# Performance work log

Hardware: AMD Instinct MI355X
Metric: run time of the kernel (lower is better)

Reference implementation:

```python
import jax, jax.numpy as jnp
from jax import lax
import numpy as np

# Quantization constants (would come from the torch state dict)
IN_S = 1.0 / 255.0   # input_scale
IN_ZP = 0            # input_zp
W_S  = [0.02, 0.02, 0.02, 0.02, 0.02, 0.02, 0.02]   # per-layer w_scale
W_ZP = [128, 128, 128, 128, 128, 128, 128]           # per-layer w_zp
OUT_S  = [0.05, 0.04, 0.04, 0.04, 0.04, 0.04, 0.05]  # per-layer act out_scale
OUT_ZP = [0, 0, 0, 0, 0, 0, 0]
PADS = [2, 0, 1, 1, 1, 1, 0]
WT_SCALE = 0.02  # last_part.w_scale used to dequantize the transpose-conv weight
DN = ('NCHW', 'OIHW', 'NCHW')


def qconv(x, w, b, in_s, in_zp, w_s, w_zp, out_s, out_zp, pad):
    # fake-quantize activation to uint8 range, shift by zero point
    xq = jnp.clip(jnp.round(x / in_s) + in_zp, 0.0, 255.0) - in_zp
    wq = w.astype(jnp.float32) - w_zp
    y = lax.conv_general_dilated(xq, wq, (1, 1), [(pad, pad), (pad, pad)],
                                 dimension_numbers=DN)
    y = y + b.astype(jnp.float32)[None, :, None, None]   # int32 accumulator bias
    # requantize to int8 range, dequantize, relu
    yq = jnp.clip(jnp.round(y * (in_s * w_s / out_s)), -127.0, 127.0)
    return jax.nn.relu((yq - out_zp) * out_s)


def deconv(x, wt):
    # torch ConvTranspose2d(16,1,k=9,stride=4,padding=4,bias=False)
    # equivalent: lhs-dilated conv with flipped, transposed kernel, pad = k-1-p = 4
    k = jnp.flip(jnp.transpose(wt, (1, 0, 2, 3)), axis=(2, 3))  # (O=1, I=16, 9, 9)
    return lax.conv_general_dilated(x, k, (1, 1), [(4, 4), (4, 4)],
                                    lhs_dilation=(4, 4), dimension_numbers=DN)


def setup_inputs() -> dict:
    key = jax.random.key(0)
    ks = jax.random.split(key, 20)
    shapes_w = [(16, 1, 5, 5), (12, 16, 1, 1), (12, 12, 3, 3), (12, 12, 3, 3),
                (12, 12, 3, 3), (12, 12, 3, 3), (16, 12, 1, 1)]
    inp = {"x": jax.random.uniform(ks[0], (16, 1, 512, 512), dtype=jnp.float32)}
    for i, sh in enumerate(shapes_w):
        inp[f"w{i}"] = jax.random.randint(ks[1 + i], sh, 0, 256, dtype=jnp.int32)
        inp[f"b{i}"] = jax.random.randint(ks[8 + i], (sh[0],), 0, 512, dtype=jnp.int32)
    # dequantized transpose-conv weight: int8-ish values * w_scale
    inp["wt"] = jax.random.normal(ks[15], (16, 1, 9, 9), dtype=jnp.float32) * WT_SCALE
    return inp


def reference(x, w0, w1, w2, w3, w4, w5, w6,
              b0, b1, b2, b3, b4, b5, b6, wt):
    ws = [w0, w1, w2, w3, w4, w5, w6]
    bs = [b0, b1, b2, b3, b4, b5, b6]
    cur_s, cur_zp = IN_S, IN_ZP
    for i in range(7):
        x = qconv(x, ws[i], bs[i], cur_s, cur_zp,
                  W_S[i], W_ZP[i], OUT_S[i], OUT_ZP[i], PADS[i])
        cur_s, cur_zp = OUT_S[i], OUT_ZP[i]
    return deconv(x, wt)
```

## Files before the change

### kernel.cpp

```cpp
#include <hip/hip_runtime.h>
#include <stdint.h>

typedef unsigned int uint;
typedef float f2 __attribute__((ext_vector_type(2)));
#define DEV __device__ __forceinline__


DEV int dot4(uint a, uint b, int c) {
#if __has_builtin(__builtin_amdgcn_sdot4)
    return __builtin_amdgcn_sdot4((int)a, (int)b, c, false);
#else
    int r = c;
    r += (int)(int8_t)(a)       * (int)(int8_t)(b);
    r += (int)(int8_t)(a >> 8)  * (int)(int8_t)(b >> 8);
    r += (int)(int8_t)(a >> 16) * (int)(int8_t)(b >> 16);
    r += (int)(int8_t)(a >> 24) * (int)(int8_t)(b >> 24);
    return r;
#endif
}

DEV uint alignbyte(uint hi, uint lo, int m) {
#if __has_builtin(__builtin_amdgcn_alignbyte)
    return __builtin_amdgcn_alignbyte(hi, lo, m);
#else
    return (uint)((((uint64_t)hi << 32) | (uint64_t)lo) >> (8 * m));
#endif
}

DEV uint requant_relu(int acc, float M) {
    float q = rintf((float)acc * M);
    q = fminf(fmaxf(q, -127.f), 127.f);
    q = fmaxf(q, 0.f);
    return (uint)q;
}

__global__ __launch_bounds__(256) void k_quant(const float* __restrict__ x,
                                               uint8_t* __restrict__ xq,
                                               float in_s) {
    int i = blockIdx.x * 256 + threadIdx.x;
    float4 v = ((const float4*)x)[i];
    uint b0 = (uint)fminf(fmaxf(rintf(v.x / in_s), 0.f), 255.f);
    uint b1 = (uint)fminf(fmaxf(rintf(v.y / in_s), 0.f), 255.f);
    uint b2 = (uint)fminf(fmaxf(rintf(v.z / in_s), 0.f), 255.f);
    uint b3 = (uint)fminf(fmaxf(rintf(v.w / in_s), 0.f), 255.f);
    ((uint*)xq)[i] = b0 | (b1 << 8) | (b2 << 16) | (b3 << 24);
}

__global__ __launch_bounds__(256) void k_l0(const uint8_t* __restrict__ xq,
                                            const int* __restrict__ w,
                                            const int* __restrict__ b,
                                            uint8_t* __restrict__ out, float M) {
    __shared__ uint tin[5][68];
    __shared__ uint wrow[5][16];
    __shared__ uint w4p[16];
    __shared__ int  w44[16];
    __shared__ int  beff[16];
    int t  = threadIdx.x;
    int x0 = blockIdx.x * 256;
    int y  = blockIdx.y;
    int n  = blockIdx.z;
    const uint8_t* xp = xq + (size_t)n * 512 * 512;

    for (int j = t; j < 330; j += 256) {
        int r = j / 66, d = j % 66;
        int yy = y - 2 + r;
        int gb = x0 - 4 + 4 * d;
        uint v = 0;
        if ((unsigned)yy < 512u && (unsigned)gb < 512u)
            v = *(const uint*)(xp + (size_t)yy * 512 + gb);
        tin[r][d] = v;
    }
    if (t < 80) {
        int oc = t / 5, r = t % 5;
        uint pk = 0;
#pragma unroll
        for (int k = 0; k < 4; ++k) {
            int wv = w[oc * 25 + r * 5 + k] - 128;
            pk |= ((uint)(uint8_t)(int8_t)wv) << (8 * k);
        }
        wrow[r][oc] = pk;
    }
    if (t < 16) {
        uint pk = 0;
#pragma unroll
        for (int r = 0; r < 4; ++r) {
            int wv = w[t * 25 + r * 5 + 4] - 128;
            pk |= ((uint)(uint8_t)(int8_t)wv) << (8 * r);
        }
        w4p[t] = pk;
        w44[t] = w[t * 25 + 24] - 128;
        int s = 0;
        for (int p = 0; p < 25; ++p) s += w[t * 25 + p] - 128;
        beff[t] = b[t] + 128 * s;
    }
    __syncthreads();

    int m  = (t + 2) & 3;
    int d0 = (t + 2) >> 2;
    uint e0[5], t4[5];
#pragma unroll
    for (int r = 0; r < 5; ++r) {
        uint a0 = tin[r][d0], a1 = tin[r][d0 + 1];
        e0[r] = alignbyte(a1, a0, m) ^ 0x80808080u;
        t4[r] = (a1 >> (8 * m)) & 0xffu;
    }
    uint lo4 = (t4[0] | (t4[1] << 8) | (t4[2] << 16) | (t4[3] << 24)) ^ 0x80808080u;
    int  e44 = (int)(int8_t)(uint8_t)(t4[4] ^ 0x80u);

    int acc[16];
#pragma unroll
    for (int oc = 0; oc < 16; ++oc) acc[oc] = beff[oc];
#pragma unroll
    for (int r = 0; r < 5; ++r)
#pragma unroll
        for (int oc = 0; oc < 16; ++oc) acc[oc] = dot4(e0[r], wrow[r][oc], acc[oc]);
#pragma unroll
    for (int oc = 0; oc < 16; ++oc) {
        acc[oc] = dot4(lo4, w4p[oc], acc[oc]);
        acc[oc] += e44 * w44[oc];
    }

    uint dw[4];
#pragma unroll
    for (int g = 0; g < 4; ++g) {
        uint d = 0;
#pragma unroll
        for (int k = 0; k < 4; ++k) d |= requant_relu(acc[g * 4 + k], M) << (8 * k);
        dw[g] = d;
    }
    size_t pix = (size_t)(n * 512 + y) * 512 + (x0 + t);
    ((uint4*)out)[pix] = make_uint4(dw[0], dw[1], dw[2], dw[3]);
}

template <int IC, int OC>
__global__ __launch_bounds__(256) void k_1x1(const uint8_t* __restrict__ in,
                                             const int* __restrict__ w,
                                             const int* __restrict__ b,
                                             uint8_t* __restrict__ out, float M) {
    constexpr int ICD = IC / 4;
    constexpr int OCD = OC / 4;
    __shared__ uint wl[OC * ICD];
    __shared__ int  bl[OC];
    int t = threadIdx.x;
    for (int j = t; j < OC * ICD; j += 256) {
        int oc = j / ICD, d = j % ICD;
        uint pk = 0;
#pragma unroll
        for (int k = 0; k < 4; ++k) {
            int wv = w[oc * IC + d * 4 + k] - 128;
            pk |= ((uint)(uint8_t)(int8_t)wv) << (8 * k);
        }
        wl[j] = pk;
    }
    if (t < OC) bl[t] = b[t];
    __syncthreads();
    size_t pix = (size_t)blockIdx.x * 256 + t;
    uint a[ICD];
#pragma unroll
    for (int d = 0; d < ICD; ++d) a[d] = ((const uint*)in)[pix * ICD + d];
    uint dws[OCD];
#pragma unroll
    for (int g = 0; g < OCD; ++g) {
        uint dword = 0;
#pragma unroll
        for (int k = 0; k < 4; ++k) {
            int oc = g * 4 + k;
            int acc = bl[oc];
#pragma unroll
            for (int d = 0; d < ICD; ++d) acc = dot4(a[d], wl[oc * ICD + d], acc);
            dword |= requant_relu(acc, M) << (8 * k);
        }
        dws[g] = dword;
    }
#pragma unroll
    for (int g = 0; g < OCD; ++g) ((uint*)out)[pix * OCD + g] = dws[g];
}

__global__ __launch_bounds__(128) void k_3x3(const uint8_t* __restrict__ in,
                                             const int* __restrict__ w,
                                             const int* __restrict__ b,
                                             uint8_t* __restrict__ out, float M) {
    __shared__ uint wl[324];
    __shared__ int  bl[12];
    int t = threadIdx.x;
    for (int j = t; j < 324; j += 128) {
        int pos = j / 36;
        int oc  = (j % 36) / 3;
        int d   = j % 3;
        uint pk = 0;
#pragma unroll
        for (int k = 0; k < 4; ++k) {
            int ic = d * 4 + k;
            int wv = w[oc * 108 + ic * 9 + pos] - 128;
            pk |= ((uint)(uint8_t)(int8_t)wv) << (8 * k);
        }
        wl[j] = pk;
    }
    if (t < 12) bl[t] = b[t];
    __syncthreads();

    int y = blockIdx.x, n = blockIdx.y;
    int x0 = t * 4;
    const uint* ip = (const uint*)in;

    uint inr[3][6][3];
#pragma unroll
    for (int r = 0; r < 3; ++r) {
        int yy = y - 1 + r;
        bool yok = (unsigned)yy < 512u;
#pragma unroll
        for (int cidx = 0; cidx < 6; ++cidx) {
            int xx = x0 - 1 + cidx;
            bool ok = yok && (unsigned)xx < 512u;
            size_t base = ((size_t)(n * 512 + yy) * 512 + xx) * 3;
#pragma unroll
            for (int d = 0; d < 3; ++d) inr[r][cidx][d] = ok ? ip[base + d] : 0u;
        }
    }

    int acc[4][12];
#pragma unroll
    for (int p = 0; p < 4; ++p)
#pragma unroll
        for (int oc = 0; oc < 12; ++oc) acc[p][oc] = bl[oc];

#pragma unroll
    for (int ry = 0; ry < 3; ++ry) {
#pragma unroll
        for (int rx = 0; rx < 3; ++rx) {
            int pos = ry * 3 + rx;
            const uint4* wq = (const uint4*)&wl[pos * 36];
#pragma unroll
            for (int g = 0; g < 3; ++g) {
                uint4 wA = wq[g * 3 + 0];
                uint4 wB = wq[g * 3 + 1];
                uint4 wC = wq[g * 3 + 2];
                uint wocd[4][3] = {{wA.x, wA.y, wA.z}, {wA.w, wB.x, wB.y},
                                   {wB.z, wB.w, wC.x}, {wC.y, wC.z, wC.w}};
#pragma unroll
                for (int k = 0; k < 4; ++k) {
                    int oc = g * 4 + k;
#pragma unroll
                    for (int p = 0; p < 4; ++p) {
                        acc[p][oc] = dot4(inr[ry][rx + p][0], wocd[k][0], acc[p][oc]);
                        acc[p][oc] = dot4(inr[ry][rx + p][1], wocd[k][1], acc[p][oc]);
                        acc[p][oc] = dot4(inr[ry][rx + p][2], wocd[k][2], acc[p][oc]);
                    }
                }
            }
        }
    }

#pragma unroll
    for (int p = 0; p < 4; ++p) {
        uint dws[3];
#pragma unroll
        for (int g = 0; g < 3; ++g) {
            uint dword = 0;
#pragma unroll
            for (int k = 0; k < 4; ++k) dword |= requant_relu(acc[p][g * 4 + k], M) << (8 * k);
            dws[g] = dword;
        }
        size_t pix = (size_t)(n * 512 + y) * 512 + (x0 + p);
        uint* op = (uint*)out;
        op[pix * 3 + 0] = dws[0];
        op[pix * 3 + 1] = dws[1];
        op[pix * 3 + 2] = dws[2];
    }
}

__global__ __launch_bounds__(256) void k_wprep(const float* __restrict__ wt,
                                               float* __restrict__ wp) {
    int idx = blockIdx.x * 256 + threadIdx.x;
    if (idx < 2304) {
        int o = idx & 15, c = (idx >> 4) & 15, pos = idx >> 8;
        int r = pos / 3, s = pos % 3;
        int py = o >> 2, px = o & 3;
        int jy = 4 * r - py, jx = 4 * s - px;
        float v = 0.f;
        if (jy >= 0 && jy < 9 && jx >= 0 && jx < 9)
            v = wt[c * 81 + (8 - jy) * 9 + (8 - jx)];
        wp[idx] = v;
    } else if (idx < 2496) {
        int i2 = idx - 2304;
        int r = i2 >> 6, c = (i2 >> 2) & 15, py = i2 & 3;
        int jy = 4 * r - py;
        float v = 0.f;
        if (jy >= 0 && jy < 9)
            v = wt[c * 81 + (8 - jy) * 9 + 8];
        wp[idx] = v;
    }
}

template <bool ALLPY>
DEV void dc_row5(const float* __restrict__ wrow,
                 const float* __restrict__ w0tab,
                 const uint4* w3, f2* accA, f2* accB) {
    {
        uint wv[4] = {w3[0].x, w3[0].y, w3[0].z, w3[0].w};
#pragma unroll
        for (int c = 0; c < 16; ++c) {
            float x = (float)((wv[c >> 2] >> ((c & 3) * 8)) & 0xffu);
            if (ALLPY) {
                float4 w = *(const float4*)(w0tab + c * 4);
                accA[0].x = fmaf(w.x, x, accA[0].x);
                accA[1].x = fmaf(w.y, x, accA[1].x);
                accA[2].x = fmaf(w.z, x, accA[2].x);
                accA[3].x = fmaf(w.w, x, accA[3].x);
            } else {
                accA[0].x = fmaf(w0tab[c * 4], x, accA[0].x);
            }
        }
    }
#pragma unroll
    for (int s = 1; s < 3; ++s) {
        const float* wb = wrow + s * 256;
        uint wv[4] = {w3[s].x, w3[s].y, w3[s].z, w3[s].w};
#pragma unroll
        for (int c = 0; c < 16; ++c) {
            float x = (float)((wv[c >> 2] >> ((c & 3) * 8)) & 0xffu);
            f2 xx = {x, x};
#pragma unroll
            for (int py = 0; py < (ALLPY ? 4 : 1); ++py) {
                float4 w = *(const float4*)(wb + c * 16 + py * 4);
                f2 wlo = {w.x, w.y};
                f2 whi = {w.z, w.w};
                accA[py] = __builtin_elementwise_fma(wlo, xx, accA[py]);
                accB[py] = __builtin_elementwise_fma(whi, xx, accB[py]);
            }
        }
    }
}

__global__ __launch_bounds__(256, 2) void k_deconv5(const uint8_t* __restrict__ in,
                                                    const float* __restrict__ wp,
                                                    float* __restrict__ out,
                                                    float out_s) {
    __shared__ float wl[2304];
    __shared__ float wl0[192];
    int t = threadIdx.x;
#pragma unroll
    for (int j = 0; j < 9; ++j) wl[j * 256 + t] = wp[j * 256 + t];
    if (t < 192) wl0[t] = wp[2304 + t];
    __syncthreads();

    int tx = blockIdx.x * 256 + t;
    int ty = blockIdx.y;
    int n  = blockIdx.z;
    const uint4* ip = (const uint4*)in + (size_t)n * 512 * 512;

    f2 accA[4], accB[4];
#pragma unroll
    for (int i = 0; i < 4; ++i) { accA[i] = (f2){0.f, 0.f}; accB[i] = (f2){0.f, 0.f}; }

    {
        int iy = ty - 1;
        uint4 w3[3];
#pragma unroll
        for (int s = 0; s < 3; ++s) {
            int ix = tx - 1 + s;
            bool ok = (iy >= 0) && ((unsigned)ix < 512u);
            w3[s] = ok ? ip[(size_t)iy * 512 + ix] : make_uint4(0u, 0u, 0u, 0u);
        }
        dc_row5<false>(&wl[0], &wl0[0], w3, accA, accB);
    }
#pragma unroll 1
    for (int r = 1; r < 3; ++r) {
        int iy = ty - 1 + r;
        uint4 w3[3];
#pragma unroll
        for (int s = 0; s < 3; ++s) {
            int ix = tx - 1 + s;
            bool ok = (iy < 512) && ((unsigned)ix < 512u);
            w3[s] = ok ? ip[(size_t)iy * 512 + ix] : make_uint4(0u, 0u, 0u, 0u);
        }
        dc_row5<true>(&wl[r * 768], &wl0[r * 64], w3, accA, accB);
    }

    int oy0 = 4 * ty, ox0 = 4 * tx;
    float* op = out + (size_t)n * 2045 * 2045;
    int xlim = 2045 - ox0; if (xlim > 4) xlim = 4;
#pragma unroll
    for (int py = 0; py < 4; ++py) {
        int oy = oy0 + py;
        if (oy >= 2045) break;
        size_t rb = (size_t)oy * 2045 + ox0;
        float va[4] = {accA[py].x * out_s, accA[py].y * out_s,
                       accB[py].x * out_s, accB[py].y * out_s};
#pragma unroll
        for (int px = 0; px < 4; ++px) {
            if (px >= xlim) break;
            op[rb + px] = va[px];
        }
    }
}

extern "C" void kernel_launch(void* const* d_in, const int* in_sizes, int n_in,
                              void* d_out, int out_size, void* d_ws, size_t ws_size,
                              hipStream_t stream) {
    const float* x  = (const float*)d_in[0];
    const int*   w0 = (const int*)d_in[1];
    const int*   b0 = (const int*)d_in[2];
    const int*   w1 = (const int*)d_in[3];
    const int*   b1 = (const int*)d_in[4];
    const int*   w2 = (const int*)d_in[5];
    const int*   b2 = (const int*)d_in[6];
    const int*   w3 = (const int*)d_in[7];
    const int*   b3 = (const int*)d_in[8];
    const int*   w4 = (const int*)d_in[9];
    const int*   b4 = (const int*)d_in[10];
    const int*   w5 = (const int*)d_in[11];
    const int*   b5 = (const int*)d_in[12];
    const int*   w6 = (const int*)d_in[13];
    const int*   b6 = (const int*)d_in[14];
    const float* wt = (const float*)d_in[15];
    float* out = (float*)d_out;

    uint8_t* A  = (uint8_t*)d_ws;
    uint8_t* B  = (uint8_t*)d_ws + (size_t)(64 << 20);
    uint8_t* xq = B;
    float*  wpD = (float*)(B + (size_t)(60 << 20));

    const float M0  = (float)((1.0 / 255.0) * 0.02 / 0.05);
    const float M1  = (float)(0.05 * 0.02 / 0.04);
    const float M25 = (float)(0.04 * 0.02 / 0.04);
    const float M6  = (float)(0.04 * 0.02 / 0.05);
    const float IN_S_F = (float)(1.0 / 255.0);

    k_wprep<<<10, 256, 0, stream>>>(wt, wpD);
    k_quant<<<4096, 256, 0, stream>>>(x, xq, IN_S_F);
    k_l0<<<dim3(2, 512, 16), 256, 0, stream>>>(xq, w0, b0, A, M0);
    k_1x1<16, 12><<<16384, 256, 0, stream>>>(A, w1, b1, B, M1);
    k_3x3<<<dim3(512, 16), 128, 0, stream>>>(B, w2, b2, A, M25);
    k_3x3<<<dim3(512, 16), 128, 0, stream>>>(A, w3, b3, B, M25);
    k_3x3<<<dim3(512, 16), 128, 0, stream>>>(B, w4, b4, A, M25);
    k_3x3<<<dim3(512, 16), 128, 0, stream>>>(A, w5, b5, B, M25);
    k_1x1<12, 16><<<16384, 256, 0, stream>>>(B, w6, b6, A, M6);
    k_deconv5<<<dim3(2, 512, 16), 256, 0, stream>>>(A, wpD, out, 0.05f);
}
```

Before: 559.3 us.

## Fuse 1x1 convs into neighbouring kernels and widen deconv per-thread tile

The first 1x1 conv is folded into the 5x5 layer-0 kernel, and the final 1x1 conv is folded into the last 3x3 kernel through a template flag. This removes two launches and two full intermediate activation round trips through global memory. The transpose-conv kernel now has each thread compute two adjacent input columns, giving 8 output pixels per row. That reuses overlapping input loads and halves the grid, at the cost of higher register pressure.

```diff
diff --git a/kernel.cpp b/kernel.cpp
--- a/kernel.cpp
+++ b/kernel.cpp
@@ -27,6 +27,8 @@
 #endif
 }
 
+DEV float bytef(uint v, int k) { return (float)((v >> (8 * k)) & 0xffu); }
+
 DEV uint requant_relu(int acc, float M) {
     float q = rintf((float)acc * M);
     q = fminf(fmaxf(q, -127.f), 127.f);
@@ -49,12 +51,16 @@
 __global__ __launch_bounds__(256) void k_l0(const uint8_t* __restrict__ xq,
                                             const int* __restrict__ w,
                                             const int* __restrict__ b,
-                                            uint8_t* __restrict__ out, float M) {
+                                            uint8_t* __restrict__ out, float M,
+                                            const int* __restrict__ w1,
+                                            const int* __restrict__ b1, float M1) {
     __shared__ uint tin[5][68];
     __shared__ uint wrow[5][16];
     __shared__ uint w4p[16];
     __shared__ int  w44[16];
     __shared__ int  beff[16];
+    __shared__ uint w1l[48];
+    __shared__ int  b1l[12];
     int t  = threadIdx.x;
     int x0 = blockIdx.x * 256;
     int y  = blockIdx.y;
@@ -93,6 +99,17 @@
         for (int p = 0; p < 25; ++p) s += w[t * 25 + p] - 128;
         beff[t] = b[t] + 128 * s;
     }
+    if (t < 48) {
+        int oc = t >> 2, d = t & 3;
+        uint pk = 0;
+#pragma unroll
+        for (int k = 0; k < 4; ++k) {
+            int wv = w1[oc * 16 + d * 4 + k] - 128;
+            pk |= ((uint)(uint8_t)(int8_t)wv) << (8 * k);
+        }
+        w1l[t] = pk;
+    }
+    if (t >= 64 && t < 76) b1l[t - 64] = b1[t - 64];
     __syncthreads();
 
     int m  = (t + 2) & 3;
@@ -128,60 +145,35 @@
         for (int k = 0; k < 4; ++k) d |= requant_relu(acc[g * 4 + k], M) << (8 * k);
         dw[g] = d;
     }
+
     size_t pix = (size_t)(n * 512 + y) * 512 + (x0 + t);
-    ((uint4*)out)[pix] = make_uint4(dw[0], dw[1], dw[2], dw[3]);
-}
-
-template <int IC, int OC>
-__global__ __launch_bounds__(256) void k_1x1(const uint8_t* __restrict__ in,
-                                             const int* __restrict__ w,
-                                             const int* __restrict__ b,
-                                             uint8_t* __restrict__ out, float M) {
-    constexpr int ICD = IC / 4;
-    constexpr int OCD = OC / 4;
-    __shared__ uint wl[OC * ICD];
-    __shared__ int  bl[OC];
-    int t = threadIdx.x;
-    for (int j = t; j < OC * ICD; j += 256) {
-        int oc = j / ICD, d = j % ICD;
-        uint pk = 0;
-#pragma unroll
-        for (int k = 0; k < 4; ++k) {
-            int wv = w[oc * IC + d * 4 + k] - 128;
-            pk |= ((uint)(uint8_t)(int8_t)wv) << (8 * k);
-        }
-        wl[j] = pk;
-    }
-    if (t < OC) bl[t] = b[t];
-    __syncthreads();
-    size_t pix = (size_t)blockIdx.x * 256 + t;
-    uint a[ICD];
-#pragma unroll
-    for (int d = 0; d < ICD; ++d) a[d] = ((const uint*)in)[pix * ICD + d];
-    uint dws[OCD];
-#pragma unroll
-    for (int g = 0; g < OCD; ++g) {
+    uint* op = (uint*)out;
+#pragma unroll
+    for (int g = 0; g < 3; ++g) {
         uint dword = 0;
 #pragma unroll
         for (int k = 0; k < 4; ++k) {
             int oc = g * 4 + k;
-            int acc = bl[oc];
-#pragma unroll
-            for (int d = 0; d < ICD; ++d) acc = dot4(a[d], wl[oc * ICD + d], acc);
-            dword |= requant_relu(acc, M) << (8 * k);
-        }
-        dws[g] = dword;
-    }
-#pragma unroll
-    for (int g = 0; g < OCD; ++g) ((uint*)out)[pix * OCD + g] = dws[g];
-}
-
+            int a2 = b1l[oc];
+#pragma unroll
+            for (int d = 0; d < 4; ++d) a2 = dot4(dw[d], w1l[oc * 4 + d], a2);
+            dword |= requant_relu(a2, M1) << (8 * k);
+        }
+        op[pix * 3 + g] = dword;
+    }
+}
+
+template <bool FUSE>
 __global__ __launch_bounds__(128) void k_3x3(const uint8_t* __restrict__ in,
                                              const int* __restrict__ w,
                                              const int* __restrict__ b,
-                                             uint8_t* __restrict__ out, float M) {
+                                             uint8_t* __restrict__ out, float M,
+                                             const int* __restrict__ w6,
+                                             const int* __restrict__ b6, float M6) {
     __shared__ uint wl[324];
     __shared__ int  bl[12];
+    __shared__ uint w6l[48];
+    __shared__ int  b6l[16];
     int t = threadIdx.x;
     for (int j = t; j < 324; j += 128) {
         int pos = j / 36;
@@ -197,6 +189,19 @@
         wl[j] = pk;
     }
     if (t < 12) bl[t] = b[t];
+    if (FUSE) {
+        if (t >= 16 && t < 64) {
+            int j = t - 16, oc = j / 3, d = j % 3;
+            uint pk = 0;
+#pragma unroll
+            for (int k = 0; k < 4; ++k) {
+                int wv = w6[oc * 12 + d * 4 + k] - 128;
+                pk |= ((uint)(uint8_t)(int8_t)wv) << (8 * k);
+            }
+            w6l[j] = pk;
+        }
+        if (t >= 64 && t < 80) b6l[t - 64] = b6[t - 64];
+    }
     __syncthreads();
 
     int y = blockIdx.x, n = blockIdx.y;
@@ -262,10 +267,28 @@
             dws[g] = dword;
         }
         size_t pix = (size_t)(n * 512 + y) * 512 + (x0 + p);
-        uint* op = (uint*)out;
-        op[pix * 3 + 0] = dws[0];
-        op[pix * 3 + 1] = dws[1];
-        op[pix * 3 + 2] = dws[2];
+        if (!FUSE) {
+            uint* op = (uint*)out;
+            op[pix * 3 + 0] = dws[0];
+            op[pix * 3 + 1] = dws[1];
+            op[pix * 3 + 2] = dws[2];
+        } else {
+            uint dw2[4];
+#pragma unroll
+            for (int g = 0; g < 4; ++g) {
+                uint dword = 0;
+#pragma unroll
+                for (int k = 0; k < 4; ++k) {
+                    int oc = g * 4 + k;
+                    int a2 = b6l[oc];
+#pragma unroll
+                    for (int d = 0; d < 3; ++d) a2 = dot4(dws[d], w6l[oc * 3 + d], a2);
+                    dword |= requant_relu(a2, M6) << (8 * k);
+                }
+                dw2[g] = dword;
+            }
+            ((uint4*)out)[pix] = make_uint4(dw2[0], dw2[1], dw2[2], dw2[3]);
+        }
     }
 }
 
@@ -293,46 +316,57 @@
 }
 
 template <bool ALLPY>
-DEV void dc_row5(const float* __restrict__ wrow,
+DEV void dc_row6(const float* __restrict__ wrow,
                  const float* __restrict__ w0tab,
-                 const uint4* w3, f2* accA, f2* accB) {
-    {
-        uint wv[4] = {w3[0].x, w3[0].y, w3[0].z, w3[0].w};
-#pragma unroll
-        for (int c = 0; c < 16; ++c) {
-            float x = (float)((wv[c >> 2] >> ((c & 3) * 8)) & 0xffu);
-            if (ALLPY) {
-                float4 w = *(const float4*)(w0tab + c * 4);
-                accA[0].x = fmaf(w.x, x, accA[0].x);
-                accA[1].x = fmaf(w.y, x, accA[1].x);
-                accA[2].x = fmaf(w.z, x, accA[2].x);
-                accA[3].x = fmaf(w.w, x, accA[3].x);
-            } else {
-                accA[0].x = fmaf(w0tab[c * 4], x, accA[0].x);
-            }
+                 const uint4* ld,
+                 f2 (&accA)[2][4], f2 (&accB)[2][4]) {
+    uint bv[4][4];
+#pragma unroll
+    for (int s = 0; s < 4; ++s) { bv[s][0] = ld[s].x; bv[s][1] = ld[s].y; bv[s][2] = ld[s].z; bv[s][3] = ld[s].w; }
+#pragma unroll
+    for (int c = 0; c < 16; ++c) {
+        float xA = bytef(bv[0][c >> 2], c & 3);
+        float xB = bytef(bv[1][c >> 2], c & 3);
+        if (ALLPY) {
+            float4 wv = *(const float4*)(w0tab + c * 4);
+            accA[0][0].x = fmaf(wv.x, xA, accA[0][0].x);
+            accA[0][1].x = fmaf(wv.y, xA, accA[0][1].x);
+            accA[0][2].x = fmaf(wv.z, xA, accA[0][2].x);
+            accA[0][3].x = fmaf(wv.w, xA, accA[0][3].x);
+            accA[1][0].x = fmaf(wv.x, xB, accA[1][0].x);
+            accA[1][1].x = fmaf(wv.y, xB, accA[1][1].x);
+            accA[1][2].x = fmaf(wv.z, xB, accA[1][2].x);
+            accA[1][3].x = fmaf(wv.w, xB, accA[1][3].x);
+        } else {
+            float w0 = w0tab[c * 4];
+            accA[0][0].x = fmaf(w0, xA, accA[0][0].x);
+            accA[1][0].x = fmaf(w0, xB, accA[1][0].x);
         }
     }
 #pragma unroll
     for (int s = 1; s < 3; ++s) {
         const float* wb = wrow + s * 256;
-        uint wv[4] = {w3[s].x, w3[s].y, w3[s].z, w3[s].w};
 #pragma unroll
         for (int c = 0; c < 16; ++c) {
-            float x = (float)((wv[c >> 2] >> ((c & 3) * 8)) & 0xffu);
-            f2 xx = {x, x};
+            float xA = bytef(bv[s][c >> 2], c & 3);
+            float xB = bytef(bv[s + 1][c >> 2], c & 3);
+            f2 xxA = {xA, xA};
+            f2 xxB = {xB, xB};
 #pragma unroll
             for (int py = 0; py < (ALLPY ? 4 : 1); ++py) {
-                float4 w = *(const float4*)(wb + c * 16 + py * 4);
-                f2 wlo = {w.x, w.y};
-                f2 whi = {w.z, w.w};
-                accA[py] = __builtin_elementwise_fma(wlo, xx, accA[py]);
-                accB[py] = __builtin_elementwise_fma(whi, xx, accB[py]);
+                float4 wv = *(const float4*)(wb + c * 16 + py * 4);
+                f2 wlo = {wv.x, wv.y};
+                f2 whi = {wv.z, wv.w};
+                accA[0][py] = __builtin_elementwise_fma(wlo, xxA, accA[0][py]);
+                accB[0][py] = __builtin_elementwise_fma(whi, xxA, accB[0][py]);
+                accA[1][py] = __builtin_elementwise_fma(wlo, xxB, accA[1][py]);
+                accB[1][py] = __builtin_elementwise_fma(whi, xxB, accB[1][py]);
             }
         }
     }
 }
 
-__global__ __launch_bounds__(256, 2) void k_deconv5(const uint8_t* __restrict__ in,
+__global__ __launch_bounds__(256, 2) void k_deconv6(const uint8_t* __restrict__ in,
                                                     const float* __restrict__ wp,
                                                     float* __restrict__ out,
                                                     float out_s) {
@@ -344,51 +378,55 @@
     if (t < 192) wl0[t] = wp[2304 + t];
     __syncthreads();
 
-    int tx = blockIdx.x * 256 + t;
+    int gx = t;
     int ty = blockIdx.y;
     int n  = blockIdx.z;
     const uint4* ip = (const uint4*)in + (size_t)n * 512 * 512;
 
-    f2 accA[4], accB[4];
-#pragma unroll
-    for (int i = 0; i < 4; ++i) { accA[i] = (f2){0.f, 0.f}; accB[i] = (f2){0.f, 0.f}; }
+    f2 accA[2][4], accB[2][4];
+#pragma unroll
+    for (int k = 0; k < 2; ++k)
+#pragma unroll
+        for (int i = 0; i < 4; ++i) { accA[k][i] = (f2){0.f, 0.f}; accB[k][i] = (f2){0.f, 0.f}; }
 
     {
         int iy = ty - 1;
-        uint4 w3[3];
-#pragma unroll
-        for (int s = 0; s < 3; ++s) {
-            int ix = tx - 1 + s;
+        uint4 ld[4];
+#pragma unroll
+        for (int s = 0; s < 4; ++s) {
+            int ix = 2 * gx - 1 + s;
             bool ok = (iy >= 0) && ((unsigned)ix < 512u);
-            w3[s] = ok ? ip[(size_t)iy * 512 + ix] : make_uint4(0u, 0u, 0u, 0u);
-        }
-        dc_row5<false>(&wl[0], &wl0[0], w3, accA, accB);
+            ld[s] = ok ? ip[(size_t)iy * 512 + ix] : make_uint4(0u, 0u, 0u, 0u);
+        }
+        dc_row6<false>(&wl[0], &wl0[0], ld, accA, accB);
     }
 #pragma unroll 1
     for (int r = 1; r < 3; ++r) {
         int iy = ty - 1 + r;
-        uint4 w3[3];
-#pragma unroll
-        for (int s = 0; s < 3; ++s) {
-            int ix = tx - 1 + s;
+        uint4 ld[4];
+#pragma unroll
+        for (int s = 0; s < 4; ++s) {
+            int ix = 2 * gx - 1 + s;
             bool ok = (iy < 512) && ((unsigned)ix < 512u);
-            w3[s] = ok ? ip[(size_t)iy * 512 + ix] : make_uint4(0u, 0u, 0u, 0u);
-        }
-        dc_row5<true>(&wl[r * 768], &wl0[r * 64], w3, accA, accB);
-    }
-
-    int oy0 = 4 * ty, ox0 = 4 * tx;
+            ld[s] = ok ? ip[(size_t)iy * 512 + ix] : make_uint4(0u, 0u, 0u, 0u);
+        }
+        dc_row6<true>(&wl[r * 768], &wl0[r * 64], ld, accA, accB);
+    }
+
+    int oy0 = 4 * ty, ox0 = 8 * gx;
     float* op = out + (size_t)n * 2045 * 2045;
-    int xlim = 2045 - ox0; if (xlim > 4) xlim = 4;
+    int xlim = 2045 - ox0; if (xlim > 8) xlim = 8;
 #pragma unroll
     for (int py = 0; py < 4; ++py) {
         int oy = oy0 + py;
         if (oy >= 2045) break;
         size_t rb = (size_t)oy * 2045 + ox0;
-        float va[4] = {accA[py].x * out_s, accA[py].y * out_s,
-                       accB[py].x * out_s, accB[py].y * out_s};
-#pragma unroll
-        for (int px = 0; px < 4; ++px) {
+        float va[8] = {accA[0][py].x * out_s, accA[0][py].y * out_s,
+                       accB[0][py].x * out_s, accB[0][py].y * out_s,
+                       accA[1][py].x * out_s, accA[1][py].y * out_s,
+                       accB[1][py].x * out_s, accB[1][py].y * out_s};
+#pragma unroll
+        for (int px = 0; px < 8; ++px) {
             if (px >= xlim) break;
             op[rb + px] = va[px];
         }
@@ -429,12 +467,10 @@
 
     k_wprep<<<10, 256, 0, stream>>>(wt, wpD);
     k_quant<<<4096, 256, 0, stream>>>(x, xq, IN_S_F);
-    k_l0<<<dim3(2, 512, 16), 256, 0, stream>>>(xq, w0, b0, A, M0);
-    k_1x1<16, 12><<<16384, 256, 0, stream>>>(A, w1, b1, B, M1);
-    k_3x3<<<dim3(512, 16), 128, 0, stream>>>(B, w2, b2, A, M25);
-    k_3x3<<<dim3(512, 16), 128, 0, stream>>>(A, w3, b3, B, M25);
-    k_3x3<<<dim3(512, 16), 128, 0, stream>>>(B, w4, b4, A, M25);
-    k_3x3<<<dim3(512, 16), 128, 0, stream>>>(A, w5, b5, B, M25);
-    k_1x1<12, 16><<<16384, 256, 0, stream>>>(B, w6, b6, A, M6);
-    k_deconv5<<<dim3(2, 512, 16), 256, 0, stream>>>(A, wpD, out, 0.05f);
-}
+    k_l0<<<dim3(2, 512, 16), 256, 0, stream>>>(xq, w0, b0, A, M0, w1, b1, M1);
+    k_3x3<false><<<dim3(512, 16), 128, 0, stream>>>(A, w2, b2, B, M25, nullptr, nullptr, 0.f);
+    k_3x3<false><<<dim3(512, 16), 128, 0, stream>>>(B, w3, b3, A, M25, nullptr, nullptr, 0.f);
+    k_3x3<false><<<dim3(512, 16), 128, 0, stream>>>(A, w4, b4, B, M25, nullptr, nullptr, 0.f);
+    k_3x3<true><<<dim3(512, 16), 128, 0, stream>>>(B, w5, b5, A, M25, w6, b6, M6);
+    k_deconv6<<<dim3(1, 512, 16), 256, 0, stream>>>(A, wpD, out, 0.05f);
+}
```

Result: faster. 518.4 us (-7.3%).
